# Performance work log

Measured on AMD Instinct MI355X. Metric: run time of the kernel, lower is better.

Reference implementation:

```python
import jax, jax.numpy as jnp
import numpy as np
import math

R = 16            # input_resolution (window side)
N = R * R         # tokens per window
H = 16            # num_heads
D = 32            # head_dim
SCALE = D ** -0.5

def _rel_pos_index(r):
    # Swin-style relative position index, [N, N] int
    coords = np.stack(np.meshgrid(np.arange(r), np.arange(r), indexing='ij'))  # [2,r,r]
    cf = coords.reshape(2, -1)                          # [2, N]
    rel = cf[:, :, None] - cf[:, None, :]               # [2, N, N]
    rel = rel.transpose(1, 2, 0).astype(np.int64)       # [N, N, 2]
    rel[:, :, 0] += r - 1
    rel[:, :, 1] += r - 1
    rel[:, :, 0] *= 2 * r - 1
    return rel.sum(-1)                                  # [N, N]

def _modulation(n, k):
    # cosine-distance modulation matrix, [n*n, n*n]
    idx = np.arange(n * n)
    rr, cc = idx // n, idx % n
    d = np.sqrt((rr[:, None] - rr[None, :]) ** 2 + (cc[:, None] - cc[None, :]) ** 2)
    T = 4 * (n - 1) * math.sqrt(2)
    f = 2 * math.pi / T
    m = np.exp(np.cos(f * d)) / 2
    if k % n == 0:
        k = k - 1
    bound = m[0, k]
    m = np.where(m < bound, 0.0, m)
    return jnp.asarray(m, jnp.float32)

_REL_IDX = jnp.asarray(_rel_pos_index(R))   # [N, N] int
_MOD = _modulation(R, 3 * R)                 # [N, N] float (eval-mode local modulation)

def setup_inputs() -> dict:
    key = jax.random.key(0)
    ks = jax.random.split(key, 6)
    C = H * D
    return {
        'x': jax.random.normal(ks[0], (128, N, C), jnp.float32),
        'qkv_w': jax.random.normal(ks[1], (3 * C, C), jnp.float32) * 0.02,
        'qkv_b': jax.random.normal(ks[2], (3 * C,), jnp.float32) * 0.02,
        'proj_w': jax.random.normal(ks[3], (C, C), jnp.float32) * 0.02,
        'proj_b': jax.random.normal(ks[4], (C,), jnp.float32) * 0.02,
        'rpb_table': jax.random.normal(ks[5], ((2 * R - 1) ** 2, H), jnp.float32) * 0.02,
    }

def reference(x, qkv_w, qkv_b, proj_w, proj_b, rpb_table):
    B, n, C = x.shape
    # qkv projection: torch Linear is x @ W^T + b
    qkv = x @ qkv_w.T + qkv_b                       # [B, N, 3C]
    qkv = qkv.reshape(B, n, 3, H, D)
    q = qkv[:, :, 0].transpose(0, 2, 1, 3) * SCALE  # [B, H, N, D]
    k = qkv[:, :, 1].transpose(0, 2, 1, 3)
    v = qkv[:, :, 2].transpose(0, 2, 1, 3)
    attn = jnp.einsum('bhnd,bhmd->bhnm', q, k)      # [B, H, N, N]
    bias = rpb_table[_REL_IDX]                      # [N, N, H]
    attn = attn + bias.transpose(2, 0, 1)[None]     # + [1, H, N, N]
    attn = jax.nn.softmax(attn, axis=-1)
    attn = attn * _MOD[None, None]                  # local eval-mode modulation
    out = jnp.einsum('bhnm,bhmd->bhnd', attn, v)    # [B, H, N, D]
    out = out.transpose(0, 2, 1, 3).reshape(B, n, C)
    return out @ proj_w.T + proj_b
```

## Files before the change

### kernel.cpp

```cpp
#include <hip/hip_runtime.h>
#include <hip/hip_bf16.h>

typedef unsigned short u16;
typedef unsigned int u32;
typedef __bf16 bf16x8 __attribute__((ext_vector_type(8)));
typedef float f32x4 __attribute__((ext_vector_type(4)));

#define AS1(p) ((const __attribute__((address_space(1))) void*)(p))
#define AS3(p) ((__attribute__((address_space(3))) void*)(p))

#define TOK   256
#define CDIM  512
#define QKVC  1536
#define LOG2E 1.4426950408889634f
#define QSCALE (0.17677669529663687f * 1.4426950408889634f)

__device__ __forceinline__ u16 f2b(float f) {
  unsigned u = __float_as_uint(f);
  unsigned r = (u + 0x7fffu + ((u >> 16) & 1u)) >> 16;
  return (u16)r;
}
__device__ __forceinline__ u16 f2bc(float f) {
  __bf16 h = (__bf16)f;
  u16 u;
  __builtin_memcpy(&u, &h, 2);
  return u;
}
__device__ __forceinline__ float bf_lo(u32 wd) { return __uint_as_float(wd << 16); }
__device__ __forceinline__ float bf_hi(u32 wd) { return __uint_as_float(wd & 0xffff0000u); }
__device__ __forceinline__ float ex2(float x) {
  float r;
  asm("v_exp_f32 %0, %1" : "=v"(r) : "v"(x));
  return r;
}

__global__ __launch_bounds__(256) void cvt_bf16_kernel(const float* __restrict__ in,
                                                       u16* __restrict__ out, int n) {
  int i = (blockIdx.x * 256 + threadIdx.x) * 8;
  if (i >= n) return;
  float4 a = *(const float4*)(in + i);
  float4 b = *(const float4*)(in + i + 4);
  u16 h[8];
  h[0] = f2b(a.x); h[1] = f2b(a.y); h[2] = f2b(a.z); h[3] = f2b(a.w);
  h[4] = f2b(b.x); h[5] = f2b(b.y); h[6] = f2b(b.z); h[7] = f2b(b.w);
  *(uint4*)(out + i) = *(const uint4*)h;
}

__global__ __launch_bounds__(256) void build_bias2_kernel(const float* __restrict__ rpb,
                                                          u16* __restrict__ bias2) {
  int i = blockIdx.x * 256 + threadIdx.x;
  int tr = i & 63, lane = (i >> 6) & 63, rb = (i >> 12) & 15, h = i >> 16;
  int t = tr >> 2, r = tr & 3;
  int n = rb * 16 + (lane & 15);
  int m = t * 16 + (lane >> 4) * 4 + r;
  int idx = ((n >> 4) - (m >> 4) + 15) * 31 + ((n & 15) - (m & 15) + 15);
  bias2[i] = f2b(rpb[idx * 16 + h] * LOG2E);
}

__global__ __launch_bounds__(256) void build_mod2_kernel(u16* __restrict__ mod2) {
  int i = blockIdx.x * 256 + threadIdx.x;
  int tr = i & 63, lane = (i >> 6) & 63, rb = i >> 12;
  int t = tr >> 2, r = tr & 3;
  int n = rb * 16 + (lane & 15);
  int m = t * 16 + (lane >> 4) * 4 + r;
  int dr = (n >> 4) - (m >> 4), dc = (n & 15) - (m & 15);
  int d2 = dr * dr + dc * dc;
  float val = 0.0f;
  if (d2 <= 229) {
    const float fc = 6.2831853071795864f / (60.0f * 1.4142135623730951f);
    val = expf(cosf(fc * sqrtf((float)d2))) * 0.5f;
  }
  mod2[i] = f2b(val);
}

template<int MODE>
__global__ __launch_bounds__(256) void gemm_bt(const u16* __restrict__ A,
                                               const u16* __restrict__ Bt,
                                               const float* __restrict__ bvec,
                                               u16* __restrict__ oq,
                                               u16* __restrict__ ok,
                                               u16* __restrict__ ov,
                                               float* __restrict__ of) {
  constexpr int K = 512;
  constexpr int NBN = (MODE == 0) ? 12 : 4;
  constexpr int PER_XCD = (MODE == 0) ? 384 : 128;
  __shared__ __align__(16) u16 As[128 * 64];
  __shared__ __align__(16) u16 Bs[128 * 64];
  const int tid = threadIdx.x, lane = tid & 63, w = tid >> 6;
  const int wr = w >> 1, wc = w & 1, lr = lane & 15, lg = lane >> 4;
  const int logical = (blockIdx.x & 7) * PER_XCD + (blockIdx.x >> 3);
  const int bm = (logical / (2 * NBN)) * 2 + (logical & 1);
  const int bn = (logical % (2 * NBN)) >> 1;
  const u16* Ag = A + (size_t)bm * 128 * K;
  const u16* Bg = Bt + (size_t)bn * 128 * K;
  f32x4 acc[4][4];
#pragma unroll
  for (int m = 0; m < 4; ++m)
#pragma unroll
    for (int n = 0; n < 4; ++n) acc[m][n] = (f32x4){0.f, 0.f, 0.f, 0.f};

  for (int k0 = 0; k0 < K; k0 += 64) {
#pragma unroll
    for (int it = 0; it < 4; ++it) {
      int chunk = it * 256 + w * 64 + lane;
      int r = chunk >> 3, kc = chunk & 7;
      int kcs = kc ^ (r & 7);
      __builtin_amdgcn_global_load_lds(AS1(Ag + (size_t)r * K + k0 + kcs * 8),
                                       AS3(As + chunk * 8), 16, 0, 0);
      __builtin_amdgcn_global_load_lds(AS1(Bg + (size_t)r * K + k0 + kcs * 8),
                                       AS3(Bs + chunk * 8), 16, 0, 0);
    }
    __syncthreads();
#pragma unroll
    for (int kk = 0; kk < 2; ++kk) {
      bf16x8 a[4], b[4];
#pragma unroll
      for (int m = 0; m < 4; ++m) {
        int ar = wr * 64 + m * 16 + lr;
        a[m] = *(const bf16x8*)&As[ar * 64 + (((kk * 4 + lg) ^ (lr & 7)) << 3)];
      }
#pragma unroll
      for (int n = 0; n < 4; ++n) {
        int br = wc * 64 + n * 16 + lr;
        b[n] = *(const bf16x8*)&Bs[br * 64 + (((kk * 4 + lg) ^ (lr & 7)) << 3)];
      }
#pragma unroll
      for (int m = 0; m < 4; ++m)
#pragma unroll
        for (int n = 0; n < 4; ++n)
          acc[m][n] = __builtin_amdgcn_mfma_f32_16x16x32_bf16(a[m], b[n], acc[m][n], 0, 0, 0);
    }
    __syncthreads();
  }

  if (MODE == 1) {
#pragma unroll
    for (int m = 0; m < 4; ++m)
#pragma unroll
      for (int n = 0; n < 4; ++n)
#pragma unroll
        for (int r = 0; r < 4; ++r) {
          int row = bm * 128 + wr * 64 + m * 16 + lg * 4 + r;
          int col = bn * 128 + wc * 64 + n * 16 + lr;
          of[(size_t)row * CDIM + col] = acc[m][n][r] + bvec[col];
        }
    return;
  }

  const int typ = bn >> 2;
  const int col0 = bn * 128 + wc * 64;
  const int row0 = bm * 128 + wr * 64;
  char* Tb = (char*)((w < 2 ? As : Bs) + (w & 1) * 4096);

#pragma unroll
  for (int n = 0; n < 4; ++n) {
    float bv = bvec[col0 + n * 16 + lr];
#pragma unroll
    for (int m = 0; m < 4; ++m)
#pragma unroll
      for (int r = 0; r < 4; ++r) {
        float v = acc[m][n][r] + bv;
        if (typ == 0) v *= QSCALE;
        int row_l, col_l;
        if (typ < 2) { row_l = m * 16 + lg * 4 + r; col_l = n * 16 + lr; }
        else         { row_l = n * 16 + lr;         col_l = m * 16 + lg * 4 + r; }
        int byte = row_l * 128 + ((((col_l >> 3) ^ (row_l & 7)) << 4) | ((col_l & 7) << 1));
        *(u16*)(Tb + byte) = f2b(v);
      }
  }
  if (typ < 2) {
    int tok = row0 + lane;
    int tokb = tok >> 8;
    u16* obase = (typ == 0) ? oq : ok;
#pragma unroll
    for (int G = 0; G < 8; ++G) {
      int hl = G >> 2, q = G & 3;
      uint4 v = *(const uint4*)(Tb + lane * 128 + ((G ^ (lane & 7)) << 4));
      int hh = ((col0 >> 5) & 15) + hl;
      size_t a = ((((size_t)tokb * 16 + hh) * 16 + ((tok >> 4) & 15)) * 64 +
                  ((tok & 15) | (q << 4))) * 8;
      *(uint4*)(obase + a) = v;
    }
  } else {
    int tl0 = row0 & 255, tokb = row0 >> 8;
    int hl = lane >> 5, t = (lane >> 3) & 3, c = lane & 7;
    int hh = ((col0 >> 5) & 15) + hl;
#pragma unroll
    for (int i = 0; i < 8; ++i) {
      int d = i * 4 + t;
      uint4 v = *(const uint4*)(Tb + (hl * 32 + d) * 128 + (c << 4));
      size_t a = (((size_t)tokb * 16 + hh) * 32 + d) * 256 + tl0 + c * 8;
      *(uint4*)(ov + a) = v;
    }
  }
}

__global__ __launch_bounds__(256, 4) void attn_kernel(const u16* __restrict__ qfrag,
                                                      const u16* __restrict__ kfrag,
                                                      const u16* __restrict__ vsw,
                                                      const u16* __restrict__ bias2,
                                                      const u16* __restrict__ mod2,
                                                      u16* __restrict__ attnout) {
  __shared__ __align__(16) u16 SM[16384];
  const int logical = ((blockIdx.x & 7) << 10) + (blockIdx.x >> 3);
  const int h = logical >> 9;
  const int rem = logical & 511;
  const int b = rem >> 2, qb = rem & 3;
  const int tid = threadIdx.x, lane = tid & 63, w = tid >> 6;
  const int lr = lane & 15, lg = lane >> 4;
  const int rb = qb * 4 + w, n0 = rb * 16;
  const int bhid = b * 16 + h;

  const u16* kg = kfrag + (size_t)bhid * 8192;
  const u16* vg = vsw + (size_t)bhid * 8192;
#pragma unroll
  for (int it = 0; it < 4; ++it) {
    __builtin_amdgcn_global_load_lds(AS1(kg + (it * 256 + tid) * 8),
                                     AS3(SM + (it * 256 + tid) * 8), 16, 0, 0);
    __builtin_amdgcn_global_load_lds(AS1(vg + (it * 256 + tid) * 8),
                                     AS3(SM + 8192 + (it * 256 + tid) * 8), 16, 0, 0);
  }
  bf16x8 qf = *(const bf16x8*)(qfrag + ((size_t)bhid * 16 + rb) * 512 + lane * 8);
  u32 bw[32];
  {
    const uint4* bp = (const uint4*)(bias2 + (((size_t)h * 16 + rb) * 64 + lane) * 64);
#pragma unroll
    for (int j = 0; j < 8; ++j) *(uint4*)&bw[j * 4] = bp[j];
  }
  __syncthreads();

  f32x4 s[16];
#pragma unroll
  for (int t = 0; t < 16; ++t) {
    bf16x8 kf = *(const bf16x8*)(SM + (t * 64 + lane) * 8);
    f32x4 c;
    c[0] = bf_lo(bw[t * 2]);     c[1] = bf_hi(bw[t * 2]);
    c[2] = bf_lo(bw[t * 2 + 1]); c[3] = bf_hi(bw[t * 2 + 1]);
    s[t] = __builtin_amdgcn_mfma_f32_16x16x32_bf16(kf, qf, c, 0, 0, 0);
  }

  u32 mw[32];
  {
    const uint4* mp = (const uint4*)(mod2 + ((size_t)rb * 64 + lane) * 64);
#pragma unroll
    for (int j = 0; j < 8; ++j) *(uint4*)&mw[j * 4] = mp[j];
  }

  float mr0 = s[0][0], mr1 = s[0][1], mr2 = s[0][2], mr3 = s[0][3];
#pragma unroll
  for (int t = 1; t < 16; ++t) {
    mr0 = fmaxf(mr0, s[t][0]); mr1 = fmaxf(mr1, s[t][1]);
    mr2 = fmaxf(mr2, s[t][2]); mr3 = fmaxf(mr3, s[t][3]);
  }
  float mx = fmaxf(fmaxf(mr0, mr1), fmaxf(mr2, mr3));
  mx = fmaxf(mx, __shfl_xor(mx, 16, 64));
  mx = fmaxf(mx, __shfl_xor(mx, 32, 64));
  float s0 = 0.f, s1 = 0.f, s2 = 0.f, s3 = 0.f;
#pragma unroll
  for (int t = 0; t < 16; ++t) {
    s[t][0] = ex2(s[t][0] - mx); s0 += s[t][0];
    s[t][1] = ex2(s[t][1] - mx); s1 += s[t][1];
    s[t][2] = ex2(s[t][2] - mx); s2 += s[t][2];
    s[t][3] = ex2(s[t][3] - mx); s3 += s[t][3];
  }
  float sm = (s0 + s1) + (s2 + s3);
  sm += __shfl_xor(sm, 16, 64);
  sm += __shfl_xor(sm, 32, 64);
  sm = __builtin_amdgcn_rcpf(sm);

  __syncthreads();

  f32x4 o0 = (f32x4){0.f, 0.f, 0.f, 0.f};
  f32x4 o1 = (f32x4){0.f, 0.f, 0.f, 0.f};
  char* Pbase = (char*)SM + w * 4096;
  const char* Vb = (const char*)(SM + 8192);
#pragma unroll
  for (int half = 0; half < 2; ++half) {
#pragma unroll
    for (int tl = 0; tl < 8; ++tl) {
      int t = half * 8 + tl;
      u16 pk[4];
#pragma unroll
      for (int r = 0; r < 4; ++r) {
        u32 wd = mw[t * 2 + (r >> 1)];
        float mf = (r & 1) ? bf_hi(wd) : bf_lo(wd);
        pk[r] = f2bc(s[t][r] * sm * mf);
      }
      int hi2 = (t * 2 + (lg >> 1)) & 3;
      *(uint2*)(Pbase + ((t >> 1) & 3) * 1024 + ((hi2 << 4) | lr) * 16 + (lg & 1) * 8)
          = *(const uint2*)pk;
    }
#pragma unroll
    for (int kkr = 0; kkr < 4; ++kkr) {
      bf16x8 pa = *(const bf16x8*)(Pbase + kkr * 1024 + lane * 16);
      int cv = ((half * 4 + kkr) * 4 + lg) ^ (lr & 7);
      bf16x8 v0 = *(const bf16x8*)(Vb + lr * 512 + cv * 16);
      bf16x8 v1 = *(const bf16x8*)(Vb + (16 + lr) * 512 + cv * 16);
      o0 = __builtin_amdgcn_mfma_f32_16x16x32_bf16(pa, v0, o0, 0, 0, 0);
      o1 = __builtin_amdgcn_mfma_f32_16x16x32_bf16(pa, v1, o1, 0, 0, 0);
    }
  }
  u16* orow = attnout + (size_t)(b * TOK + n0) * CDIM + h * 32;
#pragma unroll
  for (int r = 0; r < 4; ++r) {
    orow[(size_t)(lg * 4 + r) * CDIM + lr] = f2bc(o0[r]);
    orow[(size_t)(lg * 4 + r) * CDIM + 16 + lr] = f2bc(o1[r]);
  }
}

extern "C" void kernel_launch(void* const* d_in, const int* in_sizes, int n_in,
                              void* d_out, int out_size, void* d_ws, size_t ws_size,
                              hipStream_t stream) {
  const float* x      = (const float*)d_in[0];
  const float* qkv_w  = (const float*)d_in[1];
  const float* qkv_b  = (const float*)d_in[2];
  const float* proj_w = (const float*)d_in[3];
  const float* proj_b = (const float*)d_in[4];
  const float* rpb    = (const float*)d_in[5];

  char* ws = (char*)d_ws;
  u16* xb     = (u16*)(ws);
  u16* qkvwb  = (u16*)(ws + 33554432);
  u16* projwb = (u16*)(ws + 35127296);
  u16* qfrag  = (u16*)(ws + 35651584);
  u16* kfrag  = (u16*)(ws + 69206016);
  u16* vswb   = (u16*)(ws + 102760448);
  u16* attnb  = (u16*)(ws + 136314880);
  u16* bias2  = (u16*)(ws + 169869312);
  u16* mod2   = (u16*)(ws + 171966464);

  cvt_bf16_kernel<<<8192, 256, 0, stream>>>(x, xb, 32768 * 512);
  cvt_bf16_kernel<<<384, 256, 0, stream>>>(qkv_w, qkvwb, 1536 * 512);
  cvt_bf16_kernel<<<128, 256, 0, stream>>>(proj_w, projwb, 512 * 512);
  build_bias2_kernel<<<4096, 256, 0, stream>>>(rpb, bias2);
  build_mod2_kernel<<<256, 256, 0, stream>>>(mod2);

  gemm_bt<0><<<3072, 256, 0, stream>>>(xb, qkvwb, qkv_b, qfrag, kfrag, vswb, nullptr);
  attn_kernel<<<8192, 256, 0, stream>>>(qfrag, kfrag, vswb, bias2, mod2, attnb);
  gemm_bt<1><<<1024, 256, 0, stream>>>(attnb, projwb, proj_b,
                                       nullptr, nullptr, nullptr, (float*)d_out);
}
```

Measured before the change: 227.7 us.

## Use 512-thread attention blocks sharing K/V across eight query row-blocks

Each attention block now runs 8 waves covering half a head's query rows, so each K/V tile is loaded into LDS once per 8 row-blocks instead of once per 4. The grid is halved. P scratch gets its own LDS region, which removes the second barrier. Bias and modulation values are streamed in chunks of 4 tiles rather than held in 32-register arrays, to cut register pressure. LDS per block grows to 48KB, which may limit how many blocks fit on a CU.

```diff
diff --git a/kernel.cpp b/kernel.cpp
--- a/kernel.cpp
+++ b/kernel.cpp
@@ -168,6 +168,7 @@
         *(u16*)(Tb + byte) = f2b(v);
       }
   }
+  asm volatile("" ::: "memory");
   if (typ < 2) {
     int tok = row0 + lane;
     int tokb = tok >> 8;
@@ -195,55 +196,56 @@
   }
 }
 
-__global__ __launch_bounds__(256, 4) void attn_kernel(const u16* __restrict__ qfrag,
+__global__ __launch_bounds__(512, 4) void attn_kernel(const u16* __restrict__ qfrag,
                                                       const u16* __restrict__ kfrag,
                                                       const u16* __restrict__ vsw,
                                                       const u16* __restrict__ bias2,
                                                       const u16* __restrict__ mod2,
                                                       u16* __restrict__ attnout) {
-  __shared__ __align__(16) u16 SM[16384];
-  const int logical = ((blockIdx.x & 7) << 10) + (blockIdx.x >> 3);
-  const int h = logical >> 9;
-  const int rem = logical & 511;
-  const int b = rem >> 2, qb = rem & 3;
+  __shared__ __align__(16) u16 SM[24576];
+  const int logical = (blockIdx.x & 7) * 512 + (blockIdx.x >> 3);
+  const int h = logical >> 8;
+  const int b = (logical >> 1) & 127;
+  const int qpair = logical & 1;
   const int tid = threadIdx.x, lane = tid & 63, w = tid >> 6;
   const int lr = lane & 15, lg = lane >> 4;
-  const int rb = qb * 4 + w, n0 = rb * 16;
+  const int rb = qpair * 8 + w;
   const int bhid = b * 16 + h;
 
   const u16* kg = kfrag + (size_t)bhid * 8192;
   const u16* vg = vsw + (size_t)bhid * 8192;
 #pragma unroll
-  for (int it = 0; it < 4; ++it) {
-    __builtin_amdgcn_global_load_lds(AS1(kg + (it * 256 + tid) * 8),
-                                     AS3(SM + (it * 256 + tid) * 8), 16, 0, 0);
-    __builtin_amdgcn_global_load_lds(AS1(vg + (it * 256 + tid) * 8),
-                                     AS3(SM + 8192 + (it * 256 + tid) * 8), 16, 0, 0);
+  for (int it = 0; it < 2; ++it) {
+    __builtin_amdgcn_global_load_lds(AS1(kg + (it * 512 + tid) * 8),
+                                     AS3(SM + (it * 512 + tid) * 8), 16, 0, 0);
+    __builtin_amdgcn_global_load_lds(AS1(vg + (it * 512 + tid) * 8),
+                                     AS3(SM + 8192 + (it * 512 + tid) * 8), 16, 0, 0);
   }
   bf16x8 qf = *(const bf16x8*)(qfrag + ((size_t)bhid * 16 + rb) * 512 + lane * 8);
-  u32 bw[32];
-  {
-    const uint4* bp = (const uint4*)(bias2 + (((size_t)h * 16 + rb) * 64 + lane) * 64);
-#pragma unroll
-    for (int j = 0; j < 8; ++j) *(uint4*)&bw[j * 4] = bp[j];
-  }
   __syncthreads();
 
+  const u16* bias_base = bias2 + (((size_t)h * 16 + rb) * 64 + lane) * 64;
+  const u16* mod_base  = mod2 + ((size_t)rb * 64 + lane) * 64;
+  char* Pbase = (char*)SM + 32768 + w * 2048;
+  const char* Vb = (const char*)(SM + 8192);
+
   f32x4 s[16];
 #pragma unroll
-  for (int t = 0; t < 16; ++t) {
-    bf16x8 kf = *(const bf16x8*)(SM + (t * 64 + lane) * 8);
-    f32x4 c;
-    c[0] = bf_lo(bw[t * 2]);     c[1] = bf_hi(bw[t * 2]);
-    c[2] = bf_lo(bw[t * 2 + 1]); c[3] = bf_hi(bw[t * 2 + 1]);
-    s[t] = __builtin_amdgcn_mfma_f32_16x16x32_bf16(kf, qf, c, 0, 0, 0);
-  }
-
-  u32 mw[32];
-  {
-    const uint4* mp = (const uint4*)(mod2 + ((size_t)rb * 64 + lane) * 64);
-#pragma unroll
-    for (int j = 0; j < 8; ++j) *(uint4*)&mw[j * 4] = mp[j];
+  for (int q = 0; q < 4; ++q) {
+    u32 bw8[8];
+    {
+      const uint4* bp = (const uint4*)(bias_base + q * 16);
+      *(uint4*)&bw8[0] = bp[0]; *(uint4*)&bw8[4] = bp[1];
+    }
+#pragma unroll
+    for (int tl = 0; tl < 4; ++tl) {
+      int t = q * 4 + tl;
+      bf16x8 kf = *(const bf16x8*)(SM + (t * 64 + lane) * 8);
+      f32x4 c;
+      c[0] = bf_lo(bw8[tl * 2]);     c[1] = bf_hi(bw8[tl * 2]);
+      c[2] = bf_lo(bw8[tl * 2 + 1]); c[3] = bf_hi(bw8[tl * 2 + 1]);
+      s[t] = __builtin_amdgcn_mfma_f32_16x16x32_bf16(kf, qf, c, 0, 0, 0);
+    }
   }
 
   float mr0 = s[0][0], mr1 = s[0][1], mr2 = s[0][2], mr3 = s[0][3];
@@ -268,39 +270,43 @@
   sm += __shfl_xor(sm, 32, 64);
   sm = __builtin_amdgcn_rcpf(sm);
 
-  __syncthreads();
-
   f32x4 o0 = (f32x4){0.f, 0.f, 0.f, 0.f};
   f32x4 o1 = (f32x4){0.f, 0.f, 0.f, 0.f};
-  char* Pbase = (char*)SM + w * 4096;
-  const char* Vb = (const char*)(SM + 8192);
-#pragma unroll
-  for (int half = 0; half < 2; ++half) {
-#pragma unroll
-    for (int tl = 0; tl < 8; ++tl) {
-      int t = half * 8 + tl;
+#pragma unroll
+  for (int q = 0; q < 4; ++q) {
+    u32 mw8[8];
+    {
+      const uint4* mp = (const uint4*)(mod_base + q * 16);
+      *(uint4*)&mw8[0] = mp[0]; *(uint4*)&mw8[4] = mp[1];
+    }
+#pragma unroll
+    for (int tl = 0; tl < 4; ++tl) {
+      int t = q * 4 + tl;
       u16 pk[4];
 #pragma unroll
       for (int r = 0; r < 4; ++r) {
-        u32 wd = mw[t * 2 + (r >> 1)];
+        u32 wd = mw8[tl * 2 + (r >> 1)];
         float mf = (r & 1) ? bf_hi(wd) : bf_lo(wd);
         pk[r] = f2bc(s[t][r] * sm * mf);
       }
       int hi2 = (t * 2 + (lg >> 1)) & 3;
-      *(uint2*)(Pbase + ((t >> 1) & 3) * 1024 + ((hi2 << 4) | lr) * 16 + (lg & 1) * 8)
+      *(uint2*)(Pbase + ((t >> 1) & 1) * 1024 + ((hi2 << 4) | lr) * 16 + (lg & 1) * 8)
           = *(const uint2*)pk;
     }
-#pragma unroll
-    for (int kkr = 0; kkr < 4; ++kkr) {
-      bf16x8 pa = *(const bf16x8*)(Pbase + kkr * 1024 + lane * 16);
-      int cv = ((half * 4 + kkr) * 4 + lg) ^ (lr & 7);
+    asm volatile("" ::: "memory");
+#pragma unroll
+    for (int kl = 0; kl < 2; ++kl) {
+      bf16x8 pa = *(const bf16x8*)(Pbase + kl * 1024 + lane * 16);
+      int cv = ((q * 2 + kl) * 4 + lg) ^ (lr & 7);
       bf16x8 v0 = *(const bf16x8*)(Vb + lr * 512 + cv * 16);
       bf16x8 v1 = *(const bf16x8*)(Vb + (16 + lr) * 512 + cv * 16);
       o0 = __builtin_amdgcn_mfma_f32_16x16x32_bf16(pa, v0, o0, 0, 0, 0);
       o1 = __builtin_amdgcn_mfma_f32_16x16x32_bf16(pa, v1, o1, 0, 0, 0);
     }
-  }
-  u16* orow = attnout + (size_t)(b * TOK + n0) * CDIM + h * 32;
+    asm volatile("" ::: "memory");
+  }
+
+  u16* orow = attnout + (size_t)(b * TOK + rb * 16) * CDIM + h * 32;
 #pragma unroll
   for (int r = 0; r < 4; ++r) {
     orow[(size_t)(lg * 4 + r) * CDIM + lr] = f2bc(o0[r]);
@@ -336,7 +342,7 @@
   build_mod2_kernel<<<256, 256, 0, stream>>>(mod2);
 
   gemm_bt<0><<<3072, 256, 0, stream>>>(xb, qkvwb, qkv_b, qfrag, kfrag, vswb, nullptr);
-  attn_kernel<<<8192, 256, 0, stream>>>(qfrag, kfrag, vswb, bias2, mod2, attnb);
+  attn_kernel<<<4096, 512, 0, stream>>>(qfrag, kfrag, vswb, bias2, mod2, attnb);
   gemm_bt<1><<<1024, 256, 0, stream>>>(attnb, projwb, proj_b,
                                        nullptr, nullptr, nullptr, (float*)d_out);
 }
```

Measured after the change: 221.1 us. -2.9%, faster.
